# Kernel tuning notes

Hardware: AMD Instinct MI355X
Metric: run time of the kernel (lower is better)

Reference implementation:

```python
import jax, jax.numpy as jnp
import numpy as np

B, S, D, H = 1, 2048, 1024, 16
DH = D // H  # 64
HID = 4 * D
EPS = 1e-5
NEG = -1.0e9


def setup_inputs() -> dict:
    key = jax.random.key(0)
    ks = jax.random.split(key, 12)
    s = 0.02
    return {
        "y": jax.random.normal(ks[0], (B, S, D), jnp.float32),
        "encoder_output": jax.random.normal(ks[1], (B, S, D), jnp.float32),
        # per-head shared projection (query_fc used for q,k,v — faithful to source bug)
        "Wq_self": jax.random.normal(ks[2], (H, D, DH), jnp.float32) * s,
        "bq_self": jax.random.normal(ks[3], (H, DH), jnp.float32) * s,
        "Wq_cross": jax.random.normal(ks[4], (H, D, DH), jnp.float32) * s,
        "bq_cross": jax.random.normal(ks[5], (H, DH), jnp.float32) * s,
        "g1": jnp.ones((D,), jnp.float32), "beta1": jnp.zeros((D,), jnp.float32),
        "g2": jnp.ones((D,), jnp.float32), "beta2": jnp.zeros((D,), jnp.float32),
        "g3": jnp.ones((D,), jnp.float32), "beta3": jnp.zeros((D,), jnp.float32),
        "w1": jax.random.normal(ks[6], (D, HID), jnp.float32) * s,
        "b1": jax.random.normal(ks[7], (HID,), jnp.float32) * s,
        "w2": jax.random.normal(ks[8], (HID, D), jnp.float32) * s,
        "b2": jax.random.normal(ks[9], (D,), jnp.float32) * s,
    }


def _layernorm(x, g, b):
    mu = jnp.mean(x, axis=-1, keepdims=True)
    var = jnp.mean((x - mu) ** 2, axis=-1, keepdims=True)
    return (x - mu) * jax.lax.rsqrt(var + EPS) * g + b


def _mha(x_q, x_kv, W, bias, causal):
    # source bug: q, k, v all use query_fc projection
    q = jnp.einsum('bsd,hde->bhse', x_q, W) + bias[None, :, None, :]
    k = jnp.einsum('bsd,hde->bhse', x_kv, W) + bias[None, :, None, :]
    v = jnp.einsum('bsd,hde->bhse', x_kv, W) + bias[None, :, None, :]
    scores = jnp.einsum('bhse,bhte->bhst', q, k) / jnp.sqrt(jnp.float32(DH))
    if causal:
        sq, sk = scores.shape[-2], scores.shape[-1]
        mask = jnp.triu(jnp.ones((sq, sk), bool), k=1)
        scores = jnp.where(mask, NEG, scores)
    p = jax.nn.softmax(scores, axis=-1)
    out = jnp.einsum('bhst,bhte->bhse', p, v)  # [B,H,S,DH]
    b, h, s, e = out.shape
    return out.transpose(0, 2, 1, 3).reshape(b, s, h * e)


def reference(y, encoder_output, Wq_self, bq_self, Wq_cross, bq_cross,
              g1, beta1, g2, beta2, g3, beta3, w1, b1, w2, b2):
    sa = _mha(y, y, Wq_self, bq_self, causal=True)
    y1 = _layernorm(y + sa, g1, beta1)
    ca = _mha(y1, encoder_output, Wq_cross, bq_cross, causal=False)
    y2 = _layernorm(y1 + ca, g2, beta2)
    ff = jnp.maximum(y2 @ w1 + b1, 0.0) @ w2 + b2
    return _layernorm(y2 + ff, g3, beta3)
```

## Files before the change

kernel.cpp:

```cpp
#include <hip/hip_runtime.h>
#include <hip/hip_bf16.h>


#define S_LEN 2048
#define DMODEL 1024
#define NHEAD 16
#define DHEAD 64
#define HIDDEN 4096

using bf16 = __hip_bfloat16;
typedef __attribute__((ext_vector_type(8))) short bf16x8;
typedef __attribute__((ext_vector_type(4))) float floatx4;

__device__ __forceinline__ void async_ld16(const void* g, void* l) {
  __builtin_amdgcn_global_load_lds(
      (const __attribute__((address_space(1))) unsigned int*)g,
      (__attribute__((address_space(3))) unsigned int*)l, 16, 0, 0);
}

__device__ __forceinline__ unsigned short f2bf_bits(float f) {
  __hip_bfloat16 b = __float2bfloat16(f);
  return *(unsigned short*)&b;
}

template <bool HEADB>
__global__ __launch_bounds__(256) void transp_bf16_kernel(
    const float* __restrict__ src0, bf16* __restrict__ dst0,
    const float* __restrict__ src1, bf16* __restrict__ dst1, int K, int N) {
  const float* src = blockIdx.z ? src1 : src0;
  bf16* dst = blockIdx.z ? dst1 : dst0;
  __shared__ float tile[32][33];
  const int tx = threadIdx.x & 31, ty = threadIdx.x >> 5;
  const int k0 = blockIdx.y * 32, n0 = blockIdx.x * 32;
#pragma unroll
  for (int i = 0; i < 4; ++i) {
    const int k = k0 + ty + i * 8;
    const int n = n0 + tx;
    size_t idx;
    if (HEADB)
      idx = (size_t)(n >> 6) * ((size_t)K * 64) + (size_t)k * 64 + (n & 63);
    else
      idx = (size_t)k * N + n;
    tile[ty + i * 8][tx] = src[idx];
  }
  __syncthreads();
#pragma unroll
  for (int i = 0; i < 4; ++i) {
    const int n = n0 + ty + i * 8;
    const int k = k0 + tx;
    dst[(size_t)n * K + k] = __float2bfloat16(tile[tx][ty + i * 8]);
  }
}

__global__ __launch_bounds__(256) void conv_bf16_kernel(
    const float* __restrict__ src0, bf16* __restrict__ dst0,
    const float* __restrict__ src1, bf16* __restrict__ dst1, int n4) {
  const float* src = blockIdx.z ? src1 : src0;
  bf16* dst = blockIdx.z ? dst1 : dst0;
  const int i = blockIdx.x * 256 + threadIdx.x;
  if (i >= n4) return;
  float4 v = ((const float4*)src)[i];
  unsigned short r[4] = {f2bf_bits(v.x), f2bf_bits(v.y), f2bf_bits(v.z), f2bf_bits(v.w)};
  ((ushort2*)dst)[i * 2] = make_ushort2(r[0], r[1]);
  ((ushort2*)dst)[i * 2 + 1] = make_ushort2(r[2], r[3]);
}

template <int BM, int BN, bool RELU, bool DUALT, typename CT>
__global__ __launch_bounds__(256) void mfma_gemm_kernel(
    const bf16* __restrict__ A0, const bf16* __restrict__ Bt0,
    const float* __restrict__ bias0, CT* __restrict__ C0,
    bf16* __restrict__ Ct0,
    const bf16* __restrict__ A1, const bf16* __restrict__ Bt1,
    const float* __restrict__ bias1, CT* __restrict__ C1,
    bf16* __restrict__ Ct1,
    int M, int N, int Kstride, int Klen) {
  const bf16* A = blockIdx.z ? A1 : A0;
  const bf16* Bt = blockIdx.z ? Bt1 : Bt0;
  const float* bias = blockIdx.z ? bias1 : bias0;
  CT* C = blockIdx.z ? C1 : C0;
  bf16* Ct = blockIdx.z ? Ct1 : Ct0;

  constexpr int MF = BM / 32;
  constexpr int NF = BN / 32;
  __shared__ __align__(16) bf16 As[BM * 32];
  __shared__ __align__(16) bf16 Bs[BN * 32];

  const int tid = threadIdx.x;
  const int wave = tid >> 6;
  const int lane = tid & 63;
  const int m0 = blockIdx.y * BM;
  const int n0 = blockIdx.x * BN;
  const int wr = wave >> 1, wc = wave & 1;

  const int srow = wave * 16 + (lane >> 2);
  const int skcol = (lane & 3) * 8;
  const bf16* agp = A + (size_t)(m0 + srow) * Kstride + skcol;
  const bf16* bgp = Bt + (size_t)(n0 + srow) * Kstride + skcol;
  char* alds = (char*)As + wave * 1024;
  char* blds = (char*)Bs + wave * 1024;

  floatx4 acc[MF][NF];
#pragma unroll
  for (int i = 0; i < MF; ++i)
#pragma unroll
    for (int j = 0; j < NF; ++j) acc[i][j] = floatx4{0.f, 0.f, 0.f, 0.f};

  const int mrow = lane & 15;
  const int kqb = (lane >> 4) * 16;

  for (int kt = 0; kt < Klen; kt += 32) {
    __syncthreads();
#pragma unroll
    for (int i = 0; i < BM / 64; ++i)
      async_ld16(agp + (size_t)(i * 64) * Kstride + kt, alds + i * 4096);
#pragma unroll
    for (int i = 0; i < BN / 64; ++i)
      async_ld16(bgp + (size_t)(i * 64) * Kstride + kt, blds + i * 4096);
    __syncthreads();

    bf16x8 af[MF], bfr[NF];
#pragma unroll
    for (int fi = 0; fi < MF; ++fi)
      af[fi] = *(const bf16x8*)((char*)As + (wr * (BM / 2) + fi * 16 + mrow) * 64 + kqb);
#pragma unroll
    for (int fj = 0; fj < NF; ++fj)
      bfr[fj] = *(const bf16x8*)((char*)Bs + (wc * (BN / 2) + fj * 16 + mrow) * 64 + kqb);
#pragma unroll
    for (int fi = 0; fi < MF; ++fi)
#pragma unroll
      for (int fj = 0; fj < NF; ++fj)
        acc[fi][fj] = __builtin_amdgcn_mfma_f32_16x16x32_bf16(
            af[fi], bfr[fj], acc[fi][fj], 0, 0, 0);
  }

  const int erow = (lane >> 4) * 4;
  const int ecol = lane & 15;
#pragma unroll
  for (int fi = 0; fi < MF; ++fi) {
#pragma unroll
    for (int fj = 0; fj < NF; ++fj) {
      const int nn = n0 + wc * (BN / 2) + fj * 16 + ecol;
      const float bv = bias ? bias[nn] : 0.0f;
      const int mmb = m0 + wr * (BM / 2) + fi * 16 + erow;
      float v[4];
#pragma unroll
      for (int r = 0; r < 4; ++r) {
        v[r] = acc[fi][fj][r] + bv;
        if (RELU) v[r] = fmaxf(v[r], 0.0f);
        if constexpr (sizeof(CT) == 2)
          C[(size_t)(mmb + r) * N + nn] = (CT)__float2bfloat16(v[r]);
        else
          C[(size_t)(mmb + r) * N + nn] = (CT)v[r];
      }
      if (DUALT) {
        ushort4 pk;
        pk.x = f2bf_bits(v[0]);
        pk.y = f2bf_bits(v[1]);
        pk.z = f2bf_bits(v[2]);
        pk.w = f2bf_bits(v[3]);
        *(ushort4*)&Ct[(size_t)nn * M + mmb] = pk;
      }
    }
  }
}

__global__ __launch_bounds__(256) void mfma_attn_kernel(
    const bf16* __restrict__ Q, const bf16* __restrict__ K,
    const bf16* __restrict__ Vt, float* __restrict__ O, int causal) {
  __shared__ __align__(16) unsigned short Kt[64 * 64];
  __shared__ __align__(16) unsigned short Vs[64 * 64];
  __shared__ unsigned short Ps[4][16][72];
  __shared__ float Al[4][16];

  const int tid = threadIdx.x;
  const int w = tid >> 6, lane = tid & 63;
  const int g = lane >> 4, c = lane & 15;
  const int h = blockIdx.y;
  const int q0 = blockIdx.x * 64;
  const int qw = q0 + w * 16;

  const bf16* qrow = Q + (size_t)(qw + c) * DMODEL + h * DHEAD + g * 8;
  const bf16x8 qf0 = *(const bf16x8*)qrow;
  const bf16x8 qf1 = *(const bf16x8*)(qrow + 32);

  const int srow = tid >> 3;
  const int schunk = (tid & 7) ^ (srow & 7);
  const bf16* kgp = K + (size_t)srow * DMODEL + h * DHEAD + schunk * 8;
  const bf16* vgp = Vt + (size_t)(h * DHEAD + srow) * S_LEN + schunk * 8;
  char* klds = (char*)Kt + w * 1024;
  char* vlds = (char*)Vs + w * 1024;

  const int kpos0 = ((g ^ (c & 7)) << 4);
  const int kpos1 = kpos0 ^ 64;

  floatx4 of[4];
#pragma unroll
  for (int md = 0; md < 4; ++md) of[md] = floatx4{0.f, 0.f, 0.f, 0.f};
  float lpart[4] = {0.f, 0.f, 0.f, 0.f};

  const int nkt = causal ? (q0 / 64 + 1) : (S_LEN / 64);
  for (int kt = 0; kt < nkt; ++kt) {
    const int t0 = kt * 64;

    __syncthreads();
    async_ld16(kgp + (size_t)t0 * DMODEL, klds);
    async_ld16(kgp + (size_t)(t0 + 32) * DMODEL, klds + 4096);
    async_ld16(vgp + t0, vlds);
    async_ld16(vgp + (size_t)32 * S_LEN + t0, vlds + 4096);
    __syncthreads();

    floatx4 sf[4];
#pragma unroll
    for (int jt = 0; jt < 4; ++jt) {
      const char* kr = (const char*)Kt + (16 * jt + c) * 128;
      const bf16x8 kf0 = *(const bf16x8*)(kr + kpos0);
      const bf16x8 kf1 = *(const bf16x8*)(kr + kpos1);
      floatx4 s = floatx4{0.f, 0.f, 0.f, 0.f};
      s = __builtin_amdgcn_mfma_f32_16x16x32_bf16(qf0, kf0, s, 0, 0, 0);
      s = __builtin_amdgcn_mfma_f32_16x16x32_bf16(qf1, kf1, s, 0, 0, 0);
      sf[jt] = s;
    }

    const bool diag = causal && (kt == nkt - 1);
#pragma unroll
    for (int jt = 0; jt < 4; ++jt) {
#pragma unroll
      for (int r = 0; r < 4; ++r) {
        float p = __expf(0.125f * sf[jt][r]);
        if (diag && (t0 + 16 * jt + c > qw + 4 * g + r)) p = 0.0f;
        lpart[r] += p;
        Ps[w][4 * g + r][16 * jt + c] = f2bf_bits(p);
      }
    }

#pragma unroll
    for (int ks = 0; ks < 2; ++ks) {
      const bf16x8 pf = *(const bf16x8*)&Ps[w][c][g * 8 + 32 * ks];
      const int vpos = ks ? kpos1 : kpos0;
#pragma unroll
      for (int md = 0; md < 4; ++md) {
        const bf16x8 vf =
            *(const bf16x8*)((const char*)Vs + (md * 16 + c) * 128 + vpos);
        of[md] = __builtin_amdgcn_mfma_f32_16x16x32_bf16(vf, pf, of[md], 0, 0, 0);
      }
    }
  }

#pragma unroll
  for (int r = 0; r < 4; ++r) {
#pragma unroll
    for (int off = 1; off < 16; off <<= 1)
      lpart[r] += __shfl_xor(lpart[r], off, 64);
    if (c == 0) Al[w][4 * g + r] = lpart[r];
  }
  const float linv = 1.0f / Al[w][c];
  float* orow = O + (size_t)(qw + c) * DMODEL + h * DHEAD;
#pragma unroll
  for (int md = 0; md < 4; ++md) {
    float4 v;
    v.x = of[md][0] * linv;
    v.y = of[md][1] * linv;
    v.z = of[md][2] * linv;
    v.w = of[md][3] * linv;
    *(float4*)(orow + md * 16 + 4 * g) = v;
  }
}

template <bool DUAL, bool SUM2>
__global__ __launch_bounds__(256) void add_ln_kernel(
    const float* __restrict__ X, const float* __restrict__ R,
    const float* __restrict__ R2, const float* __restrict__ bvec,
    const float* __restrict__ g, const float* __restrict__ beta,
    float* __restrict__ out, bf16* __restrict__ out2) {
  const int row = blockIdx.x;
  const int tid = threadIdx.x;

  float v[4];
  float s1 = 0.0f, s2 = 0.0f;
#pragma unroll
  for (int i = 0; i < 4; ++i) {
    const int c = tid + i * 256;
    float x = X[(size_t)row * DMODEL + c] + R[(size_t)row * DMODEL + c];
    if (SUM2) x += R2[(size_t)row * DMODEL + c] + bvec[c];
    v[i] = x;
    s1 += x;
    s2 += x * x;
  }
#pragma unroll
  for (int off = 32; off; off >>= 1) {
    s1 += __shfl_xor(s1, off, 64);
    s2 += __shfl_xor(s2, off, 64);
  }
  __shared__ float w1s[4], w2s[4];
  const int wid = tid >> 6, lane = tid & 63;
  if (lane == 0) { w1s[wid] = s1; w2s[wid] = s2; }
  __syncthreads();
  s1 = w1s[0] + w1s[1] + w1s[2] + w1s[3];
  s2 = w2s[0] + w2s[1] + w2s[2] + w2s[3];

  const float mu = s1 * (1.0f / DMODEL);
  const float var = s2 * (1.0f / DMODEL) - mu * mu;
  const float rstd = rsqrtf(var + 1e-5f);

#pragma unroll
  for (int i = 0; i < 4; ++i) {
    const int c = tid + i * 256;
    const float r = (v[i] - mu) * rstd * g[c] + beta[c];
    out[(size_t)row * DMODEL + c] = r;
    if (DUAL) out2[(size_t)row * DMODEL + c] = __float2bfloat16(r);
  }
}

extern "C" void kernel_launch(void* const* d_in, const int* in_sizes, int n_in,
                              void* d_out, int out_size, void* d_ws, size_t ws_size,
                              hipStream_t stream) {
  const float* y      = (const float*)d_in[0];
  const float* enc    = (const float*)d_in[1];
  const float* Wself  = (const float*)d_in[2];
  const float* bself  = (const float*)d_in[3];
  const float* Wcross = (const float*)d_in[4];
  const float* bcross = (const float*)d_in[5];
  const float* g1     = (const float*)d_in[6];
  const float* be1    = (const float*)d_in[7];
  const float* g2     = (const float*)d_in[8];
  const float* be2    = (const float*)d_in[9];
  const float* g3     = (const float*)d_in[10];
  const float* be3    = (const float*)d_in[11];
  const float* w1     = (const float*)d_in[12];
  const float* b1     = (const float*)d_in[13];
  const float* w2     = (const float*)d_in[14];
  const float* b2     = (const float*)d_in[15];
  float* out = (float*)d_out;

  char* ws = (char*)d_ws;
  const size_t MB = 1024 * 1024;
  float* Y1   = (float*)(ws + 0 * MB);
  float* ATT  = (float*)(ws + 8 * MB);
  float* Y2   = (float*)(ws + 16 * MB);
  bf16*  Q12b = (bf16*)(ws + 24 * MB);
  bf16*  Q1t  = (bf16*)(ws + 28 * MB);
  bf16*  K2b  = (bf16*)(ws + 32 * MB);
  bf16*  K2t  = (bf16*)(ws + 36 * MB);
  bf16*  w1t  = (bf16*)(ws + 40 * MB);
  bf16*  w2t  = (bf16*)(ws + 48 * MB);
  bf16*  Wst  = (bf16*)(ws + 56 * MB);
  bf16*  Wct  = (bf16*)(ws + 58 * MB);
  bf16*  ybf  = (bf16*)(ws + 60 * MB);
  bf16*  Y1bf = (bf16*)(ws + 60 * MB);
  bf16*  encbf = (bf16*)(ws + 64 * MB);
  bf16*  Y2bf  = (bf16*)(ws + 64 * MB);
  bf16*  FFH  = (bf16*)(ws + 0 * MB);
  float* FFa  = (float*)(ws + 24 * MB);
  float* FFb  = (float*)(ws + 32 * MB);

  const dim3 blk(256);
  const dim3 gT_w(DMODEL / 32, DMODEL / 32, 2);
  const dim3 gT_w1(HIDDEN / 32, DMODEL / 32);
  const dim3 gT_w2(DMODEL / 32, HIDDEN / 32);
  const dim3 gConv(S_LEN * DMODEL / 4 / 256, 1, 2);
  const dim3 gProj2(DMODEL / 64, S_LEN / 64, 2);
  const dim3 gProj(DMODEL / 64, S_LEN / 64);
  const dim3 gFf1(HIDDEN / 128, S_LEN / 64);
  const dim3 gFf2(DMODEL / 64, S_LEN / 64, 2);
  const dim3 gAttn(S_LEN / 64, NHEAD);
  const dim3 gLn(S_LEN);

  transp_bf16_kernel<true><<<gT_w, blk, 0, stream>>>(
      Wself, Wst, Wcross, Wct, DMODEL, DMODEL);
  transp_bf16_kernel<false><<<gT_w1, blk, 0, stream>>>(
      w1, w1t, nullptr, nullptr, DMODEL, HIDDEN);
  transp_bf16_kernel<false><<<gT_w2, blk, 0, stream>>>(
      w2, w2t, nullptr, nullptr, HIDDEN, DMODEL);
  conv_bf16_kernel<<<gConv, blk, 0, stream>>>(
      y, ybf, enc, encbf, S_LEN * DMODEL / 4);

  mfma_gemm_kernel<64, 64, false, true, bf16><<<gProj2, blk, 0, stream>>>(
      ybf, Wst, bself, Q12b, Q1t,
      encbf, Wct, bcross, K2b, K2t, S_LEN, DMODEL, DMODEL, DMODEL);
  mfma_attn_kernel<<<gAttn, blk, 0, stream>>>(Q12b, Q12b, Q1t, ATT, 1);
  add_ln_kernel<true, false><<<gLn, blk, 0, stream>>>(
      y, ATT, nullptr, nullptr, g1, be1, Y1, Y1bf);
  mfma_gemm_kernel<64, 64, false, false, bf16><<<gProj, blk, 0, stream>>>(
      Y1bf, Wct, bcross, Q12b, nullptr,
      nullptr, nullptr, nullptr, nullptr, nullptr, S_LEN, DMODEL, DMODEL, DMODEL);
  mfma_attn_kernel<<<gAttn, blk, 0, stream>>>(Q12b, K2b, K2t, ATT, 0);
  add_ln_kernel<true, false><<<gLn, blk, 0, stream>>>(
      Y1, ATT, nullptr, nullptr, g2, be2, Y2, Y2bf);
  mfma_gemm_kernel<64, 128, true, false, bf16><<<gFf1, blk, 0, stream>>>(
      Y2bf, w1t, b1, FFH, nullptr,
      nullptr, nullptr, nullptr, nullptr, nullptr, S_LEN, HIDDEN, DMODEL, DMODEL);
  mfma_gemm_kernel<64, 64, false, false, float><<<gFf2, blk, 0, stream>>>(
      FFH, w2t, nullptr, FFa, nullptr,
      FFH + HIDDEN / 2, w2t + HIDDEN / 2, nullptr, FFb, nullptr,
      S_LEN, DMODEL, HIDDEN, HIDDEN / 2);
  add_ln_kernel<false, true><<<gLn, blk, 0, stream>>>(
      Y2, FFa, FFb, b2, g3, be3, out, nullptr);
}
```

Measured before the change: 347.3 us.

## Split attention KV loop across two blocks and merge partials in add-LayerNorm

Attention now runs with a grid z-dimension of 2: each block processes alternate KV tiles and writes unnormalised partial outputs plus per-row softmax denominators. The add+LayerNorm kernel gains a MERGE mode that sums the two partials and divides by the combined denominator. This doubles the number of attention blocks for better occupancy and balances the causal workload. QK^T is also transposed (K as the A operand) so exp and P stores happen per tile in vectorised form, and the row-sum reduction shrinks to two shuffles. The cost is extra partial-output memory traffic. Merging without a running max is valid only because the kernel already skips max subtraction.

```diff
diff --git a/kernel.cpp b/kernel.cpp
--- a/kernel.cpp
+++ b/kernel.cpp
@@ -166,18 +166,22 @@
 
 __global__ __launch_bounds__(256) void mfma_attn_kernel(
     const bf16* __restrict__ Q, const bf16* __restrict__ K,
-    const bf16* __restrict__ Vt, float* __restrict__ O, int causal) {
+    const bf16* __restrict__ Vt,
+    float* __restrict__ OA, float* __restrict__ OB,
+    float* __restrict__ LA, float* __restrict__ LB, int causal) {
   __shared__ __align__(16) unsigned short Kt[64 * 64];
   __shared__ __align__(16) unsigned short Vs[64 * 64];
   __shared__ unsigned short Ps[4][16][72];
-  __shared__ float Al[4][16];
 
   const int tid = threadIdx.x;
   const int w = tid >> 6, lane = tid & 63;
   const int g = lane >> 4, c = lane & 15;
   const int h = blockIdx.y;
   const int q0 = blockIdx.x * 64;
+  const int z = blockIdx.z;
   const int qw = q0 + w * 16;
+  float* Oz = z ? OB : OA;
+  float* Lz = z ? LB : LA;
 
   const bf16* qrow = Q + (size_t)(qw + c) * DMODEL + h * DHEAD + g * 8;
   const bf16x8 qf0 = *(const bf16x8*)qrow;
@@ -196,10 +200,10 @@
   floatx4 of[4];
 #pragma unroll
   for (int md = 0; md < 4; ++md) of[md] = floatx4{0.f, 0.f, 0.f, 0.f};
-  float lpart[4] = {0.f, 0.f, 0.f, 0.f};
+  float lpart = 0.0f;
 
   const int nkt = causal ? (q0 / 64 + 1) : (S_LEN / 64);
-  for (int kt = 0; kt < nkt; ++kt) {
+  for (int kt = z; kt < nkt; kt += 2) {
     const int t0 = kt * 64;
 
     __syncthreads();
@@ -209,33 +213,31 @@
     async_ld16(vgp + (size_t)32 * S_LEN + t0, vlds + 4096);
     __syncthreads();
 
-    floatx4 sf[4];
+    const bool diag = causal && (t0 == q0);
 #pragma unroll
     for (int jt = 0; jt < 4; ++jt) {
       const char* kr = (const char*)Kt + (16 * jt + c) * 128;
       const bf16x8 kf0 = *(const bf16x8*)(kr + kpos0);
       const bf16x8 kf1 = *(const bf16x8*)(kr + kpos1);
       floatx4 s = floatx4{0.f, 0.f, 0.f, 0.f};
-      s = __builtin_amdgcn_mfma_f32_16x16x32_bf16(qf0, kf0, s, 0, 0, 0);
-      s = __builtin_amdgcn_mfma_f32_16x16x32_bf16(qf1, kf1, s, 0, 0, 0);
-      sf[jt] = s;
+      s = __builtin_amdgcn_mfma_f32_16x16x32_bf16(kf0, qf0, s, 0, 0, 0);
+      s = __builtin_amdgcn_mfma_f32_16x16x32_bf16(kf1, qf1, s, 0, 0, 0);
+
+      ushort4 pk;
+      unsigned short* pp = (unsigned short*)&pk;
+#pragma unroll
+      for (int r = 0; r < 4; ++r) {
+        float p = __expf(0.125f * s[r]);
+        if (diag && (t0 + 16 * jt + 4 * g + r > qw + c)) p = 0.0f;
+        lpart += p;
+        pp[r] = f2bf_bits(p);
+      }
+      *(ushort4*)&Ps[w][c][16 * jt + 4 * g] = pk;
     }
 
-    const bool diag = causal && (kt == nkt - 1);
-#pragma unroll
-    for (int jt = 0; jt < 4; ++jt) {
-#pragma unroll
-      for (int r = 0; r < 4; ++r) {
-        float p = __expf(0.125f * sf[jt][r]);
-        if (diag && (t0 + 16 * jt + c > qw + 4 * g + r)) p = 0.0f;
-        lpart[r] += p;
-        Ps[w][4 * g + r][16 * jt + c] = f2bf_bits(p);
-      }
-    }
-
 #pragma unroll
     for (int ks = 0; ks < 2; ++ks) {
-      const bf16x8 pf = *(const bf16x8*)&Ps[w][c][g * 8 + 32 * ks];
+      const bf16x8 pf = *(const bf16x8*)&Ps[w][c][32 * ks + 8 * g];
       const int vpos = ks ? kpos1 : kpos0;
 #pragma unroll
       for (int md = 0; md < 4; ++md) {
@@ -246,30 +248,27 @@
     }
   }
 
-#pragma unroll
-  for (int r = 0; r < 4; ++r) {
-#pragma unroll
-    for (int off = 1; off < 16; off <<= 1)
-      lpart[r] += __shfl_xor(lpart[r], off, 64);
-    if (c == 0) Al[w][4 * g + r] = lpart[r];
-  }
-  const float linv = 1.0f / Al[w][c];
-  float* orow = O + (size_t)(qw + c) * DMODEL + h * DHEAD;
+  lpart += __shfl_xor(lpart, 16, 64);
+  lpart += __shfl_xor(lpart, 32, 64);
+  if (g == 0) Lz[(size_t)h * S_LEN + qw + c] = lpart;
+
+  float* orow = Oz + (size_t)(qw + c) * DMODEL + h * DHEAD;
 #pragma unroll
   for (int md = 0; md < 4; ++md) {
     float4 v;
-    v.x = of[md][0] * linv;
-    v.y = of[md][1] * linv;
-    v.z = of[md][2] * linv;
-    v.w = of[md][3] * linv;
+    v.x = of[md][0];
+    v.y = of[md][1];
+    v.z = of[md][2];
+    v.w = of[md][3];
     *(float4*)(orow + md * 16 + 4 * g) = v;
   }
 }
 
-template <bool DUAL, bool SUM2>
+template <bool DUAL, bool MERGE, bool SUM2>
 __global__ __launch_bounds__(256) void add_ln_kernel(
     const float* __restrict__ X, const float* __restrict__ R,
     const float* __restrict__ R2, const float* __restrict__ bvec,
+    const float* __restrict__ La, const float* __restrict__ Lb,
     const float* __restrict__ g, const float* __restrict__ beta,
     float* __restrict__ out, bf16* __restrict__ out2) {
   const int row = blockIdx.x;
@@ -280,8 +279,17 @@
 #pragma unroll
   for (int i = 0; i < 4; ++i) {
     const int c = tid + i * 256;
-    float x = X[(size_t)row * DMODEL + c] + R[(size_t)row * DMODEL + c];
-    if (SUM2) x += R2[(size_t)row * DMODEL + c] + bvec[c];
+    float x = X[(size_t)row * DMODEL + c];
+    if (MERGE) {
+      const int h = c >> 6;
+      const float rl =
+          1.0f / (La[(size_t)h * S_LEN + row] + Lb[(size_t)h * S_LEN + row]);
+      x += (R[(size_t)row * DMODEL + c] + R2[(size_t)row * DMODEL + c]) * rl;
+    } else if (SUM2) {
+      x += R[(size_t)row * DMODEL + c] + R2[(size_t)row * DMODEL + c] + bvec[c];
+    } else {
+      x += R[(size_t)row * DMODEL + c];
+    }
     v[i] = x;
     s1 += x;
     s2 += x * x;
@@ -334,24 +342,27 @@
 
   char* ws = (char*)d_ws;
   const size_t MB = 1024 * 1024;
-  float* Y1   = (float*)(ws + 0 * MB);
-  float* ATT  = (float*)(ws + 8 * MB);
-  float* Y2   = (float*)(ws + 16 * MB);
-  bf16*  Q12b = (bf16*)(ws + 24 * MB);
-  bf16*  Q1t  = (bf16*)(ws + 28 * MB);
-  bf16*  K2b  = (bf16*)(ws + 32 * MB);
-  bf16*  K2t  = (bf16*)(ws + 36 * MB);
-  bf16*  w1t  = (bf16*)(ws + 40 * MB);
-  bf16*  w2t  = (bf16*)(ws + 48 * MB);
-  bf16*  Wst  = (bf16*)(ws + 56 * MB);
-  bf16*  Wct  = (bf16*)(ws + 58 * MB);
-  bf16*  ybf  = (bf16*)(ws + 60 * MB);
-  bf16*  Y1bf = (bf16*)(ws + 60 * MB);
-  bf16*  encbf = (bf16*)(ws + 64 * MB);
-  bf16*  Y2bf  = (bf16*)(ws + 64 * MB);
-  bf16*  FFH  = (bf16*)(ws + 0 * MB);
-  float* FFa  = (float*)(ws + 24 * MB);
-  float* FFb  = (float*)(ws + 32 * MB);
+  bf16*  ybf   = (bf16*)(ws + 0 * MB);
+  bf16*  encbf = (bf16*)(ws + 4 * MB);
+  float* PA    = (float*)(ws + 0 * MB);
+  float* PB    = (float*)(ws + 8 * MB);
+  float* Y1    = (float*)(ws + 16 * MB);
+  float* Y2    = (float*)(ws + 24 * MB);
+  bf16*  Q12b  = (bf16*)(ws + 32 * MB);
+  bf16*  Q1t   = (bf16*)(ws + 36 * MB);
+  bf16*  K2b   = (bf16*)(ws + 40 * MB);
+  bf16*  K2t   = (bf16*)(ws + 44 * MB);
+  bf16*  w1t   = (bf16*)(ws + 48 * MB);
+  bf16*  w2t   = (bf16*)(ws + 56 * MB);
+  bf16*  Wst   = (bf16*)(ws + 64 * MB);
+  bf16*  Wct   = (bf16*)(ws + 66 * MB);
+  bf16*  Y1bf  = (bf16*)(ws + 68 * MB);
+  bf16*  Y2bf  = (bf16*)(ws + 72 * MB);
+  float* La    = (float*)(ws + 76 * MB);
+  float* Lb    = (float*)(ws + 76 * MB + 512 * 1024);
+  bf16*  FFH   = (bf16*)(ws + 0 * MB);
+  float* FFa   = (float*)(ws + 32 * MB);
+  float* FFb   = (float*)(ws + 40 * MB);
 
   const dim3 blk(256);
   const dim3 gT_w(DMODEL / 32, DMODEL / 32, 2);
@@ -362,7 +373,7 @@
   const dim3 gProj(DMODEL / 64, S_LEN / 64);
   const dim3 gFf1(HIDDEN / 128, S_LEN / 64);
   const dim3 gFf2(DMODEL / 64, S_LEN / 64, 2);
-  const dim3 gAttn(S_LEN / 64, NHEAD);
+  const dim3 gAttn(S_LEN / 64, NHEAD, 2);
   const dim3 gLn(S_LEN);
 
   transp_bf16_kernel<true><<<gT_w, blk, 0, stream>>>(
@@ -377,15 +388,17 @@
   mfma_gemm_kernel<64, 64, false, true, bf16><<<gProj2, blk, 0, stream>>>(
       ybf, Wst, bself, Q12b, Q1t,
       encbf, Wct, bcross, K2b, K2t, S_LEN, DMODEL, DMODEL, DMODEL);
-  mfma_attn_kernel<<<gAttn, blk, 0, stream>>>(Q12b, Q12b, Q1t, ATT, 1);
-  add_ln_kernel<true, false><<<gLn, blk, 0, stream>>>(
-      y, ATT, nullptr, nullptr, g1, be1, Y1, Y1bf);
+  mfma_attn_kernel<<<gAttn, blk, 0, stream>>>(
+      Q12b, Q12b, Q1t, PA, PB, La, Lb, 1);
+  add_ln_kernel<true, true, false><<<gLn, blk, 0, stream>>>(
+      y, PA, PB, nullptr, La, Lb, g1, be1, Y1, Y1bf);
   mfma_gemm_kernel<64, 64, false, false, bf16><<<gProj, blk, 0, stream>>>(
       Y1bf, Wct, bcross, Q12b, nullptr,
       nullptr, nullptr, nullptr, nullptr, nullptr, S_LEN, DMODEL, DMODEL, DMODEL);
-  mfma_attn_kernel<<<gAttn, blk, 0, stream>>>(Q12b, K2b, K2t, ATT, 0);
-  add_ln_kernel<true, false><<<gLn, blk, 0, stream>>>(
-      Y1, ATT, nullptr, nullptr, g2, be2, Y2, Y2bf);
+  mfma_attn_kernel<<<gAttn, blk, 0, stream>>>(
+      Q12b, K2b, K2t, PA, PB, La, Lb, 0);
+  add_ln_kernel<true, true, false><<<gLn, blk, 0, stream>>>(
+      Y1, PA, PB, nullptr, La, Lb, g2, be2, Y2, Y2bf);
   mfma_gemm_kernel<64, 128, true, false, bf16><<<gFf1, blk, 0, stream>>>(
       Y2bf, w1t, b1, FFH, nullptr,
       nullptr, nullptr, nullptr, nullptr, nullptr, S_LEN, HIDDEN, DMODEL, DMODEL);
@@ -393,6 +406,6 @@
       FFH, w2t, nullptr, FFa, nullptr,
       FFH + HIDDEN / 2, w2t + HIDDEN / 2, nullptr, FFb, nullptr,
       S_LEN, DMODEL, HIDDEN, HIDDEN / 2);
-  add_ln_kernel<false, true><<<gLn, blk, 0, stream>>>(
-      Y2, FFa, FFb, b2, g3, be3, out, nullptr);
-}
+  add_ln_kernel<false, false, true><<<gLn, blk, 0, stream>>>(
+      Y2, FFa, FFb, b2, nullptr, nullptr, g3, be3, out, nullptr);
+}
```

Result: faster. 325.7 us (-6.2%).
